# Optimization experiments

Measured on AMD Instinct MI355X. Metric: run time of the kernel, lower is better.

Reference implementation:

```python
import jax, jax.numpy as jnp
import numpy as np

HEADS, OUT_C = 8, 16
NEG_SLOPE = 0.2  # PyG GATConv default negative_slope


def setup_inputs() -> dict:
    key = jax.random.key(0)
    ks = jax.random.split(key, 6)
    N, E, IN = 100000, 1600000, 128
    x = jax.random.normal(ks[0], (N, IN), jnp.float32)
    edge_index = jax.random.randint(ks[1], (2, E), 0, N, dtype=jnp.int32)
    W = jax.random.normal(ks[2], (IN, HEADS * OUT_C), jnp.float32) / np.float32(np.sqrt(IN))
    att_src = jax.random.normal(ks[3], (HEADS, OUT_C), jnp.float32) * 0.1
    att_dst = jax.random.normal(ks[4], (HEADS, OUT_C), jnp.float32) * 0.1
    bias = jax.random.normal(ks[5], (HEADS * OUT_C,), jnp.float32) * 0.01
    return {"x": x, "edge_index": edge_index, "W": W,
            "att_src": att_src, "att_dst": att_dst, "bias": bias}


def reference(x, edge_index, W, att_src, att_dst, bias):
    N = x.shape[0]
    # Linear projection, split into heads: [N, H, C]
    xw = (x @ W).reshape(N, HEADS, OUT_C)
    # Add self-loops (PyG default add_self_loops=True)
    loops = jnp.arange(N, dtype=edge_index.dtype)
    src = jnp.concatenate([edge_index[0], loops])
    dst = jnp.concatenate([edge_index[1], loops])
    # Per-node attention terms [N, H], then per-edge logits
    a_s = jnp.einsum('nhc,hc->nh', xw, att_src)
    a_d = jnp.einsum('nhc,hc->nh', xw, att_dst)
    e = a_s[src] + a_d[dst]                       # [Etot, H]
    e = jnp.where(e > 0, e, NEG_SLOPE * e)        # LeakyReLU
    # Segment softmax over edges grouped by destination node
    emax = jax.ops.segment_max(e, dst, num_segments=N)
    p = jnp.exp(e - emax[dst])
    denom = jax.ops.segment_sum(p, dst, num_segments=N)
    alpha = p / (denom[dst] + 1e-16)              # [Etot, H]
    # Weighted scatter-aggregate of source messages
    out = jax.ops.segment_sum(xw[src] * alpha[:, :, None], dst, num_segments=N)
    out = out.reshape(N, HEADS * OUT_C) + bias    # concat heads + bias
    return jax.nn.relu(out)                       # act='relu', norm=None
```

## Files before the change

### kernel.cpp

```cpp
#include <hip/hip_runtime.h>
#include <math.h>

#define HEADS 8
#define OUTC 16
#define HC 128
#define NEG_SLOPE 0.2f

#define BM 128
#define BK 32
#define XPAD 132
#define CAP 64
#define EPT 8

typedef unsigned int uint;
typedef unsigned short ushort;

__device__ __forceinline__ ushort f2bf(float f) {
    uint u = __float_as_uint(f);
    u += 0x7FFFu + ((u >> 16) & 1u);
    return (ushort)(u >> 16);
}

__global__ __launch_bounds__(256, 4) void k_fused(
    const float* __restrict__ x, const float* __restrict__ W,
    const float* __restrict__ att_src, const float* __restrict__ att_dst,
    const int* __restrict__ ei,
    ushort* __restrict__ xwh, float* __restrict__ a_s, float* __restrict__ a_d,
    int* __restrict__ deg, int* __restrict__ csr,
    int N, int E, int GB, int SB) {
    __shared__ float xs[BK][XPAD];
    __shared__ float Ws[BK][XPAD];

    int bid = blockIdx.x;
    int mn = GB < SB ? GB : SB;
    int m2 = 2 * mn;
    bool is_scatter;
    int idx;
    if (bid < m2) {
        is_scatter = (bid & 1);
        idx = bid >> 1;
    } else {
        int r = bid - m2;
        is_scatter = (SB > GB);
        idx = mn + r;
    }

    if (is_scatter) {
        int base = idx * (256 * EPT) + threadIdx.x;
        int srcs[EPT], dsts[EPT], slots[EPT];
#pragma unroll
        for (int k = 0; k < EPT; ++k) {
            int e = base + k * 256;
            if (e < E) {
                srcs[k] = ei[e];
                dsts[k] = ei[E + e];
            } else {
                dsts[k] = -1;
            }
        }
#pragma unroll
        for (int k = 0; k < EPT; ++k)
            if (dsts[k] >= 0) slots[k] = atomicAdd(&deg[dsts[k]], 1);
#pragma unroll
        for (int k = 0; k < EPT; ++k)
            if (dsts[k] >= 0 && slots[k] < CAP)
                csr[(size_t)dsts[k] * CAP + slots[k]] = srcs[k];
        return;
    }

    int t = threadIdx.x;
    int nb0 = idx * BM;
    int tc = t & 15;
    int tr = t >> 4;

    float acc[8][8];
#pragma unroll
    for (int i = 0; i < 8; ++i)
#pragma unroll
        for (int j = 0; j < 8; ++j) acc[i][j] = 0.0f;

    for (int k0 = 0; k0 < HC; k0 += BK) {
        int kk4 = (t & 7) * 4;
#pragma unroll
        for (int p = 0; p < 4; ++p) {
            int nr = (t >> 3) + p * 32;
            int node = nb0 + nr;
            float4 v = make_float4(0.f, 0.f, 0.f, 0.f);
            if (node < N) v = *(const float4*)&x[(size_t)node * HC + k0 + kk4];
            xs[kk4 + 0][nr] = v.x;
            xs[kk4 + 1][nr] = v.y;
            xs[kk4 + 2][nr] = v.z;
            xs[kk4 + 3][nr] = v.w;
        }
        int kk = t >> 3;
        int c4 = (t & 7) * 4;
#pragma unroll
        for (int j = 0; j < 4; ++j) {
            *(float4*)&Ws[kk][c4 + j * 32] =
                *(const float4*)&W[(size_t)(k0 + kk) * HC + c4 + j * 32];
        }
        __syncthreads();

#pragma unroll 4
        for (int k = 0; k < BK; ++k) {
            float xa[8], wa[8];
            *(float4*)&xa[0] = *(const float4*)&xs[k][tr * 8];
            *(float4*)&xa[4] = *(const float4*)&xs[k][tr * 8 + 4];
            *(float4*)&wa[0] = *(const float4*)&Ws[k][tc * 8];
            *(float4*)&wa[4] = *(const float4*)&Ws[k][tc * 8 + 4];
#pragma unroll
            for (int i = 0; i < 8; ++i)
#pragma unroll
                for (int j = 0; j < 8; ++j)
                    acc[i][j] = fmaf(xa[i], wa[j], acc[i][j]);
        }
        __syncthreads();
    }

    float as8[8], ad8[8];
#pragma unroll
    for (int j = 0; j < 8; ++j) {
        as8[j] = att_src[tc * 8 + j];
        ad8[j] = att_dst[tc * 8 + j];
    }
    int h = tc >> 1;
#pragma unroll
    for (int i = 0; i < 8; ++i) {
        int node = nb0 + tr * 8 + i;
        float vs = 0.f, vd = 0.f;
        ushort h8[8];
#pragma unroll
        for (int j = 0; j < 8; ++j) {
            vs = fmaf(acc[i][j], as8[j], vs);
            vd = fmaf(acc[i][j], ad8[j], vd);
            h8[j] = f2bf(acc[i][j]);
        }
        vs += __shfl_xor(vs, 1);
        vd += __shfl_xor(vd, 1);
        if (node < N) {
            *(uint4*)&xwh[(size_t)node * HC + tc * 8] = *(uint4*)&h8[0];
            if ((tc & 1) == 0) {
                a_s[node * HEADS + h] = vs;
                a_d[node * HEADS + h] = vd;
            }
        }
    }
}

__global__ __launch_bounds__(256) void k_node(
    const int* __restrict__ deg, const int* __restrict__ csr,
    const float* __restrict__ a_s, const float* __restrict__ a_d,
    const uint* __restrict__ xwh, const float* __restrict__ bias,
    float* __restrict__ out, int N) {
    int n = blockIdx.x * 4 + (threadIdx.x >> 6);
    if (n >= N) return;
    int l = threadIdx.x & 63;
    int hB = l >> 3;

    float asn = a_s[n * HEADS + hB];
    float adn = a_d[n * HEADS + hB];

    float v = asn + adn;
    v = v > 0.0f ? v : NEG_SLOPE * v;
    float p = __expf(v);
    float den = p;
    uint w = xwh[n * 64 + l];
    float acc0 = p * __uint_as_float(w << 16);
    float acc1 = p * __uint_as_float(w & 0xFFFF0000u);

    int cnt = deg[n];
    if (cnt > CAP) cnt = CAP;
    const int* row = csr + (size_t)n * CAP;
#pragma unroll 4
    for (int i = 0; i < cnt; ++i) {
        int s = row[i];
        float vv = a_s[s * HEADS + hB] + adn;
        vv = vv > 0.0f ? vv : NEG_SLOPE * vv;
        float pp = __expf(vv);
        den += pp;
        uint ww = xwh[s * 64 + l];
        acc0 = fmaf(pp, __uint_as_float(ww << 16), acc0);
        acc1 = fmaf(pp, __uint_as_float(ww & 0xFFFF0000u), acc1);
    }

    float inv = 1.0f / (den + 1e-16f);
    float2 b = *(const float2*)&bias[2 * l];
    float r0 = acc0 * inv + b.x;
    float r1 = acc1 * inv + b.y;
    float2 o;
    o.x = r0 > 0.0f ? r0 : 0.0f;
    o.y = r1 > 0.0f ? r1 : 0.0f;
    *(float2*)&out[(size_t)n * HC + 2 * l] = o;
}

extern "C" void kernel_launch(void* const* d_in, const int* in_sizes, int n_in,
                              void* d_out, int out_size, void* d_ws, size_t ws_size,
                              hipStream_t stream) {
    const float* x       = (const float*)d_in[0];
    const int*   ei      = (const int*)d_in[1];
    const float* W       = (const float*)d_in[2];
    const float* att_src = (const float*)d_in[3];
    const float* att_dst = (const float*)d_in[4];
    const float* bias    = (const float*)d_in[5];
    float* out = (float*)d_out;

    int N = in_sizes[0] / HC;
    int E = in_sizes[1] / 2;

    ushort* xwh = (ushort*)d_ws;
    float* a_s  = (float*)(xwh + (size_t)N * HC);
    float* a_d  = a_s + (size_t)N * HEADS;
    int* deg    = (int*)(a_d + (size_t)N * HEADS);
    int* csr    = deg + N;

    hipMemsetAsync(deg, 0, (size_t)N * sizeof(int), stream);

    int GB = (N + BM - 1) / BM;
    int SB = (E + 256 * EPT - 1) / (256 * EPT);
    k_fused<<<GB + SB, 256, 0, stream>>>(x, W, att_src, att_dst, ei,
                                         xwh, a_s, a_d, deg, csr, N, E, GB, SB);

    k_node<<<(N + 3) / 4, 256, 0, stream>>>(deg, csr, a_s, a_d,
                                            (const uint*)xwh, bias, out, N);
}
```

Baseline: 288.2 us.

## Split fused scatter/GEMM kernel, prefetch GEMM tiles into registers, vectorize edge loads

Splits the interleaved scatter/GEMM kernel into two separate kernels launched back to back on the same stream. The GEMM now prefetches the next K-tile of x and W into registers while computing the current one, and drops the trailing barrier. The scatter kernel reads edge indices with int4 loads when E is divisible by 4. The split gives up the overlap between atomic-heavy scatter blocks and compute-bound GEMM blocks, and adds a kernel launch, in exchange for simpler kernels with register-level double buffering.

```diff
diff --git a/kernel.cpp b/kernel.cpp
--- a/kernel.cpp
+++ b/kernel.cpp
@@ -21,85 +21,109 @@
     return (ushort)(u >> 16);
 }
 
-__global__ __launch_bounds__(256, 4) void k_fused(
+__global__ __launch_bounds__(256) void k_scatter(
+    const int* __restrict__ ei, int* __restrict__ deg, int* __restrict__ csr,
+    int E) {
+    int t = threadIdx.x;
+    int base = blockIdx.x * (256 * EPT);
+    int srcs[EPT], dsts[EPT], slots[EPT];
+    bool vec = ((E & 3) == 0);
+
+#pragma unroll
+    for (int g = 0; g < EPT / 4; ++g) {
+        int eg = base + g * 1024 + 4 * t;
+        if (eg < E && vec) {
+            int4 s = *(const int4*)&ei[eg];
+            int4 d = *(const int4*)&ei[E + eg];
+            srcs[4 * g + 0] = s.x; srcs[4 * g + 1] = s.y;
+            srcs[4 * g + 2] = s.z; srcs[4 * g + 3] = s.w;
+            dsts[4 * g + 0] = d.x; dsts[4 * g + 1] = d.y;
+            dsts[4 * g + 2] = d.z; dsts[4 * g + 3] = d.w;
+        } else {
+#pragma unroll
+            for (int j = 0; j < 4; ++j) {
+                int e = eg + j;
+                if (e < E) {
+                    srcs[4 * g + j] = ei[e];
+                    dsts[4 * g + j] = ei[E + e];
+                } else {
+                    dsts[4 * g + j] = -1;
+                }
+            }
+        }
+    }
+#pragma unroll
+    for (int k = 0; k < EPT; ++k)
+        if (dsts[k] >= 0) slots[k] = atomicAdd(&deg[dsts[k]], 1);
+#pragma unroll
+    for (int k = 0; k < EPT; ++k)
+        if (dsts[k] >= 0 && slots[k] < CAP)
+            csr[(size_t)dsts[k] * CAP + slots[k]] = srcs[k];
+}
+
+__global__ __launch_bounds__(256) void k_gemm(
     const float* __restrict__ x, const float* __restrict__ W,
     const float* __restrict__ att_src, const float* __restrict__ att_dst,
-    const int* __restrict__ ei,
     ushort* __restrict__ xwh, float* __restrict__ a_s, float* __restrict__ a_d,
-    int* __restrict__ deg, int* __restrict__ csr,
-    int N, int E, int GB, int SB) {
+    int N) {
     __shared__ float xs[BK][XPAD];
     __shared__ float Ws[BK][XPAD];
 
-    int bid = blockIdx.x;
-    int mn = GB < SB ? GB : SB;
-    int m2 = 2 * mn;
-    bool is_scatter;
-    int idx;
-    if (bid < m2) {
-        is_scatter = (bid & 1);
-        idx = bid >> 1;
-    } else {
-        int r = bid - m2;
-        is_scatter = (SB > GB);
-        idx = mn + r;
-    }
-
-    if (is_scatter) {
-        int base = idx * (256 * EPT) + threadIdx.x;
-        int srcs[EPT], dsts[EPT], slots[EPT];
-#pragma unroll
-        for (int k = 0; k < EPT; ++k) {
-            int e = base + k * 256;
-            if (e < E) {
-                srcs[k] = ei[e];
-                dsts[k] = ei[E + e];
-            } else {
-                dsts[k] = -1;
-            }
-        }
-#pragma unroll
-        for (int k = 0; k < EPT; ++k)
-            if (dsts[k] >= 0) slots[k] = atomicAdd(&deg[dsts[k]], 1);
-#pragma unroll
-        for (int k = 0; k < EPT; ++k)
-            if (dsts[k] >= 0 && slots[k] < CAP)
-                csr[(size_t)dsts[k] * CAP + slots[k]] = srcs[k];
-        return;
-    }
-
     int t = threadIdx.x;
-    int nb0 = idx * BM;
+    int nb0 = blockIdx.x * BM;
     int tc = t & 15;
     int tr = t >> 4;
 
+    int kk4 = (t & 7) * 4;
+    int xr  = t >> 3;
+    int wk  = t >> 3;
+    int wc4 = (t & 7) * 4;
+
     float acc[8][8];
 #pragma unroll
     for (int i = 0; i < 8; ++i)
 #pragma unroll
         for (int j = 0; j < 8; ++j) acc[i][j] = 0.0f;
 
+    float4 xv[4], wv[4];
+
+#pragma unroll
+    for (int p = 0; p < 4; ++p) {
+        int node = nb0 + xr + p * 32;
+        xv[p] = make_float4(0.f, 0.f, 0.f, 0.f);
+        if (node < N) xv[p] = *(const float4*)&x[(size_t)node * HC + kk4];
+    }
+#pragma unroll
+    for (int j = 0; j < 4; ++j)
+        wv[j] = *(const float4*)&W[(size_t)wk * HC + wc4 + j * 32];
+
     for (int k0 = 0; k0 < HC; k0 += BK) {
-        int kk4 = (t & 7) * 4;
+        __syncthreads();
 #pragma unroll
         for (int p = 0; p < 4; ++p) {
-            int nr = (t >> 3) + p * 32;
-            int node = nb0 + nr;
-            float4 v = make_float4(0.f, 0.f, 0.f, 0.f);
-            if (node < N) v = *(const float4*)&x[(size_t)node * HC + k0 + kk4];
-            xs[kk4 + 0][nr] = v.x;
-            xs[kk4 + 1][nr] = v.y;
-            xs[kk4 + 2][nr] = v.z;
-            xs[kk4 + 3][nr] = v.w;
-        }
-        int kk = t >> 3;
-        int c4 = (t & 7) * 4;
-#pragma unroll
-        for (int j = 0; j < 4; ++j) {
-            *(float4*)&Ws[kk][c4 + j * 32] =
-                *(const float4*)&W[(size_t)(k0 + kk) * HC + c4 + j * 32];
-        }
+            int nr = xr + p * 32;
+            xs[kk4 + 0][nr] = xv[p].x;
+            xs[kk4 + 1][nr] = xv[p].y;
+            xs[kk4 + 2][nr] = xv[p].z;
+            xs[kk4 + 3][nr] = xv[p].w;
+        }
+#pragma unroll
+        for (int j = 0; j < 4; ++j)
+            *(float4*)&Ws[wk][wc4 + j * 32] = wv[j];
         __syncthreads();
+
+        int kn = k0 + BK;
+        if (kn < HC) {
+#pragma unroll
+            for (int p = 0; p < 4; ++p) {
+                int node = nb0 + xr + p * 32;
+                xv[p] = make_float4(0.f, 0.f, 0.f, 0.f);
+                if (node < N) xv[p] = *(const float4*)&x[(size_t)node * HC + kn + kk4];
+            }
+#pragma unroll
+            for (int j = 0; j < 4; ++j)
+                wv[j] = *(const float4*)&W[(size_t)(kn + wk) * HC + wc4 + j * 32];
+        }
 
 #pragma unroll 4
         for (int k = 0; k < BK; ++k) {
@@ -114,7 +138,6 @@
                 for (int j = 0; j < 8; ++j)
                     acc[i][j] = fmaf(xa[i], wa[j], acc[i][j]);
         }
-        __syncthreads();
     }
 
     float as8[8], ad8[8];
@@ -215,10 +238,11 @@
 
     hipMemsetAsync(deg, 0, (size_t)N * sizeof(int), stream);
 
+    int SB = (E + 256 * EPT - 1) / (256 * EPT);
+    k_scatter<<<SB, 256, 0, stream>>>(ei, deg, csr, E);
+
     int GB = (N + BM - 1) / BM;
-    int SB = (E + 256 * EPT - 1) / (256 * EPT);
-    k_fused<<<GB + SB, 256, 0, stream>>>(x, W, att_src, att_dst, ei,
-                                         xwh, a_s, a_d, deg, csr, N, E, GB, SB);
+    k_gemm<<<GB, 256, 0, stream>>>(x, W, att_src, att_dst, xwh, a_s, a_d, N);
 
     k_node<<<(N + 3) / 4, 256, 0, stream>>>(deg, csr, a_s, a_d,
                                             (const uint*)xwh, bias, out, N);
```

Result: slower. 358.4 us (+24.4%).
